# Optimization experiments

Hardware: AMD Instinct MI355X
Metric: run time of the kernel (lower is better)

The kernel has to match this reference:

```python
import jax, jax.numpy as jnp
import numpy as np


def _leaky(x):
    return jnp.where(x >= 0, x, 0.01 * x)  # nn.LeakyReLU default slope


def _conv1x1(x, w):
    # x: [B, C, H, W], w: [O, C] (1x1 conv == per-pixel channel GEMM)
    return jnp.einsum('bchw,oc->bohw', x, w)


def setup_inputs() -> dict:
    key = jax.random.key(0)
    ks = jax.random.split(key, 12)

    def kaiming(k, o, c):  # kaiming_normal_ fan_out, relu gain, 1x1 kernel
        return jax.random.normal(k, (o, c), jnp.float32) * np.float32(np.sqrt(2.0 / o))

    lr_feature = jax.random.normal(ks[0], (1, 32, 256, 512), jnp.float32)
    hr_feature = jax.random.normal(ks[1], (1, 32, 512, 1024), jnp.float32)
    return {
        'lr_feature': lr_feature,
        'hr_feature': hr_feature,
        's1_w0': kaiming(ks[2], 128, 128),
        's1_w1': kaiming(ks[3], 64, 128),
        's1_w2': kaiming(ks[4], 32, 64),
        's1_w3': kaiming(ks[5], 16, 32),
        's1_w4': kaiming(ks[6], 8, 16),
        's1_w5': kaiming(ks[7], 1, 8),
        's2_w0': kaiming(ks[8], 3, 3),
        's2_w1': kaiming(ks[9], 2, 3),
        's2_w2': kaiming(ks[10], 1, 2),
        'fuse_w': jnp.ones((1, 2), jnp.float32),  # fuse weight initialized to 1
    }


def reference(lr_feature, hr_feature, s1_w0, s1_w1, s1_w2, s1_w3, s1_w4, s1_w5,
              s2_w0, s2_w1, s2_w2, fuse_w):
    scale = hr_feature.shape[-1] // lr_feature.shape[-1]  # static python int (=2, even)
    Hh, Wh = hr_feature.shape[-2], hr_feature.shape[-1]

    # nearest-neighbor upsample of lr_feature by `scale` (expand/view trick in torch)
    lr_up = jnp.repeat(jnp.repeat(lr_feature, scale, axis=2), scale, axis=3)

    # representation: [B, 128, Hh, Wh]
    rep = jnp.concatenate(
        [lr_up, hr_feature, lr_up * hr_feature, (lr_up - hr_feature) ** 2], axis=1)

    # similarity_measure1: 1x1-conv MLP chain 128->128->64->32->16->8->1
    o = _leaky(_conv1x1(rep, s1_w0))
    o = _leaky(_conv1x1(o, s1_w1))
    o = _leaky(_conv1x1(o, s1_w2))
    o = _leaky(_conv1x1(o, s1_w3))
    o = _conv1x1(o, s1_w4)
    weights1 = _conv1x1(o, s1_w5)  # [B, 1, Hh, Wh]

    # distance matrix (even-scale branch): 3 channels [dx, dy, norm]
    v = jnp.arange(-(scale // 2), scale // 2 + 1, dtype=jnp.float32)
    m = v.shape[0] // 2
    v = jnp.concatenate([v[:m], v[m + 1:]])  # drop center -> length `scale`
    d0 = jnp.broadcast_to(v[None, :], (scale, scale))
    dm = jnp.stack([d0, d0.T, jnp.sqrt(d0 ** 2 + d0.T ** 2)], axis=0)  # [3,s,s]
    dm = jnp.tile(dm, (1, Hh // scale, Wh // scale))[None]  # [1, 3, Hh, Wh]

    # similarity_measure2: 3->3->2->1
    w2 = _leaky(_conv1x1(dm, s2_w0))
    w2 = _leaky(_conv1x1(w2, s2_w1))
    weights2 = _conv1x1(w2, s2_w2)  # [1, 1, Hh, Wh]

    # fuse (weight forced non-negative via abs, as in forward's .data mutation)
    mapping = _conv1x1(jnp.concatenate([weights1, weights2], axis=1), jnp.abs(fuse_w))
    return mapping
```

## Files before the change

kernel.cpp:

```cpp
#include <hip/hip_runtime.h>

typedef short v8s __attribute__((ext_vector_type(8)));
typedef float v4f __attribute__((ext_vector_type(4)));
typedef unsigned v4u __attribute__((ext_vector_type(4)));

#define Wh   1024
#define Hh   512
#define HWh  (Wh * Hh)
#define Wlr  512
#define HWlr (Wlr * 256)
#define ITERS 4
#define NBLK  1024

#define WFRAG_SHORTS (53 * 512)
#define LDS_BYTES    (WFRAG_SHORTS * 2)

__device__ __forceinline__ unsigned short f2bf(float f) {
    union { float f; unsigned u; } v; v.f = f;
    unsigned r = v.u + 0x7FFFu + ((v.u >> 16) & 1u);
    return (unsigned short)(r >> 16);
}
__device__ __forceinline__ unsigned pk2(float a, float b) {
    union { float f; unsigned u; } ua, ub;
    ua.f = a; ub.f = b;
    return __builtin_amdgcn_perm(ub.u + 0x8000u, ua.u + 0x8000u, 0x07060302u);
}
__device__ __forceinline__ float leaky(float x) { return fmaxf(x, 0.01f * x); }

__device__ __forceinline__ v8s relay(v4f e, v4f o) {
    v4u w;
    w[0] = pk2(leaky(e[0]), leaky(e[1]));
    w[1] = pk2(leaky(e[2]), leaky(e[3]));
    w[2] = pk2(leaky(o[0]), leaky(o[1]));
    w[3] = pk2(leaky(o[2]), leaky(o[3]));
    return __builtin_bit_cast(v8s, w);
}

__global__ __launch_bounds__(512, 2)
void cmfsm_kernel(const float* __restrict__ lr, const float* __restrict__ hr,
                  const float* __restrict__ w0g, const float* __restrict__ w1g,
                  const float* __restrict__ w2g, const float* __restrict__ w3g,
                  const float* __restrict__ w4g, const float* __restrict__ w5g,
                  const float* __restrict__ t0g, const float* __restrict__ t1g,
                  const float* __restrict__ t2g, const float* __restrict__ fwg,
                  float* __restrict__ out)
{
    extern __shared__ unsigned short smem[];
    unsigned short* wfrag = smem;

    const int tid  = threadIdx.x;
    const int lane = tid & 63;
    const int wv   = tid >> 6;
    const int p    = lane & 15;
    const int q    = lane >> 4;

    for (int e = tid; e < 32 * 64; e += 512) {
        int f = e >> 6, l = e & 63;
        int mt = f >> 2, ks = f & 3, pp = l & 15, qq = l >> 4;
        const float* src = w0g + (mt * 16 + pp) * 128 + ks * 32 + qq * 8;
        unsigned short* dst = wfrag + f * 512 + l * 8;
#pragma unroll
        for (int j = 0; j < 8; ++j) dst[j] = f2bf(src[j]);
    }
    for (int e = tid; e < 16 * 64; e += 512) {
        int f = e >> 6, l = e & 63;
        int mt = f >> 2, ks = f & 3, pp = l & 15, qq = l >> 4;
        const float* srcrow = w1g + (mt * 16 + pp) * 128;
        unsigned short* dst = wfrag + (32 + f) * 512 + l * 8;
#pragma unroll
        for (int j = 0; j < 8; ++j)
            dst[j] = f2bf(srcrow[ks * 32 + ((j >> 2) << 4) + qq * 4 + (j & 3)]);
    }
    if (tid < 4 * 64) {
        int f = tid >> 6, l = tid & 63;
        int mt = f >> 1, ks = f & 1, pp = l & 15, qq = l >> 4;
        const float* srcrow = w2g + (mt * 16 + pp) * 64;
        unsigned short* dst = wfrag + (48 + f) * 512 + l * 8;
#pragma unroll
        for (int j = 0; j < 8; ++j)
            dst[j] = f2bf(srcrow[ks * 32 + ((j >> 2) << 4) + qq * 4 + (j & 3)]);
    }
    if (tid < 64) {
        int l = tid;
        int pp = l & 15, qq = l >> 4;
        const float* srcrow = w3g + pp * 32;
        unsigned short* dst = wfrag + 52 * 512 + l * 8;
#pragma unroll
        for (int j = 0; j < 8; ++j)
            dst[j] = f2bf(srcrow[((j >> 2) << 4) + qq * 4 + (j & 3)]);
    }

    float w45[4];
#pragma unroll
    for (int r = 0; r < 4; ++r) {
        float s = 0.f;
#pragma unroll
        for (int j = 0; j < 8; ++j) s += w5g[j] * w4g[j * 16 + q * 4 + r];
        w45[r] = s;
    }

    const int row  = blockIdx.x >> 1;
    const int half = blockIdx.x & 1;

    float w2e, w2o;
    {
        float tab[4];
#pragma unroll
        for (int yp = 0; yp < 2; ++yp)
#pragma unroll
            for (int xp = 0; xp < 2; ++xp) {
                float i0 = xp ? 1.f : -1.f;
                float i1 = yp ? 1.f : -1.f;
                float i2 = 1.41421356237309505f;
                float h0[3], h1[2];
                for (int o = 0; o < 3; ++o)
                    h0[o] = leaky(t0g[o*3+0]*i0 + t0g[o*3+1]*i1 + t0g[o*3+2]*i2);
                for (int o = 0; o < 2; ++o)
                    h1[o] = leaky(t1g[o*3+0]*h0[0] + t1g[o*3+1]*h0[1] + t1g[o*3+2]*h0[2]);
                tab[yp*2+xp] = t2g[0]*h1[0] + t2g[1]*h1[1];
            }
        const int yp = row & 1;
        w2e = yp ? tab[2] : tab[0];
        w2o = yp ? tab[3] : tab[1];
    }
    const float fa = fabsf(fwg[0]);
    const float fb = fabsf(fwg[1]);

    __syncthreads();

    const unsigned short* WL = wfrag + lane * 8;

    const float* hrp[8];
    const float* lrp[8];
    {
        const int hbase = row * Wh + half * 512 + wv * 16 + p;
        const int lbase = (row >> 1) * Wlr + half * 256 + wv * 8 + (p >> 1);
#pragma unroll
        for (int j = 0; j < 8; ++j) {
            hrp[j] = hr + (size_t)(q * 8 + j) * HWh  + hbase;
            lrp[j] = lr + (size_t)(q * 8 + j) * HWlr + lbase;
        }
    }

    const v8s a3 = *(const v8s*)(WL + 52 * 512);

    const int obase = row * Wh + half * 512 + wv * 16 + p;

    float h[8], l[8];
#pragma unroll
    for (int j = 0; j < 8; ++j) { h[j] = hrp[j][0]; l[j] = lrp[j][0]; }

#pragma unroll
    for (int it = 0; it < ITERS; ++it) {
        v4u bf0, bf1, bf2, bf3;
#pragma unroll
        for (int u = 0; u < 4; ++u) {
            float l0 = l[2*u], l1 = l[2*u+1];
            float h0 = h[2*u], h1 = h[2*u+1];
            bf0[u] = pk2(l0, l1);
            bf1[u] = pk2(h0, h1);
            bf2[u] = pk2(l0 * h0, l1 * h1);
            float d0 = l0 - h0, d1 = l1 - h1;
            bf3[u] = pk2(d0 * d0, d1 * d1);
        }
        v8s b0 = __builtin_bit_cast(v8s, bf0);
        v8s b1 = __builtin_bit_cast(v8s, bf1);
        v8s b2 = __builtin_bit_cast(v8s, bf2);
        v8s b3 = __builtin_bit_cast(v8s, bf3);

        if (it + 1 < ITERS) {
            const int ho = (it + 1) * 128;
            const int lo = (it + 1) * 64;
#pragma unroll
            for (int j = 0; j < 8; ++j) {
                h[j] = hrp[j][ho];
                l[j] = lrp[j][lo];
            }
        }

        v8s c1[4];
#pragma unroll
        for (int ksp = 0; ksp < 4; ++ksp) {
            v4f ae = (v4f){0.f, 0.f, 0.f, 0.f};
            v4f ao = (v4f){0.f, 0.f, 0.f, 0.f};
#pragma unroll
            for (int ks = 0; ks < 4; ++ks) {
                v8s b = (ks == 0) ? b0 : (ks == 1) ? b1 : (ks == 2) ? b2 : b3;
                v8s we = *(const v8s*)(WL + ((2 * ksp)     * 4 + ks) * 512);
                v8s wo = *(const v8s*)(WL + ((2 * ksp + 1) * 4 + ks) * 512);
                ae = __builtin_amdgcn_mfma_f32_16x16x32_bf16(we, b, ae, 0, 0, 0);
                ao = __builtin_amdgcn_mfma_f32_16x16x32_bf16(wo, b, ao, 0, 0, 0);
            }
            c1[ksp] = relay(ae, ao);
        }

        v8s c2[2];
#pragma unroll
        for (int ksp = 0; ksp < 2; ++ksp) {
            v4f ae = (v4f){0.f, 0.f, 0.f, 0.f};
            v4f ao = (v4f){0.f, 0.f, 0.f, 0.f};
#pragma unroll
            for (int ks = 0; ks < 4; ++ks) {
                v8s we = *(const v8s*)(WL + (32 + (2 * ksp)     * 4 + ks) * 512);
                v8s wo = *(const v8s*)(WL + (32 + (2 * ksp + 1) * 4 + ks) * 512);
                ae = __builtin_amdgcn_mfma_f32_16x16x32_bf16(we, c1[ks], ae, 0, 0, 0);
                ao = __builtin_amdgcn_mfma_f32_16x16x32_bf16(wo, c1[ks], ao, 0, 0, 0);
            }
            c2[ksp] = relay(ae, ao);
        }

        v8s c3;
        {
            v4f ae = (v4f){0.f, 0.f, 0.f, 0.f};
            v4f ao = (v4f){0.f, 0.f, 0.f, 0.f};
#pragma unroll
            for (int ks = 0; ks < 2; ++ks) {
                v8s we = *(const v8s*)(WL + (48 +     ks) * 512);
                v8s wo = *(const v8s*)(WL + (48 + 2 + ks) * 512);
                ae = __builtin_amdgcn_mfma_f32_16x16x32_bf16(we, c2[ks], ae, 0, 0, 0);
                ao = __builtin_amdgcn_mfma_f32_16x16x32_bf16(wo, c2[ks], ao, 0, 0, 0);
            }
            c3 = relay(ae, ao);
        }

        {
            v4f acc3 = __builtin_amdgcn_mfma_f32_16x16x32_bf16(a3, c3, (v4f){0.f, 0.f, 0.f, 0.f}, 0, 0, 0);

            float part = 0.f;
#pragma unroll
            for (int r = 0; r < 4; ++r) part += w45[r] * leaky(acc3[r]);
            part += __shfl_xor(part, 16, 64);
            part += __shfl_xor(part, 32, 64);

            if (q == 0) {
                const float w2v = (p & 1) ? w2o : w2e;
                out[obase + it * 128] = fa * part + fb * w2v;
            }
        }
    }
}

extern "C" void kernel_launch(void* const* d_in, const int* in_sizes, int n_in,
                              void* d_out, int out_size, void* d_ws, size_t ws_size,
                              hipStream_t stream) {
    const float* lr  = (const float*)d_in[0];
    const float* hr  = (const float*)d_in[1];
    const float* w0g = (const float*)d_in[2];
    const float* w1g = (const float*)d_in[3];
    const float* w2g = (const float*)d_in[4];
    const float* w3g = (const float*)d_in[5];
    const float* w4g = (const float*)d_in[6];
    const float* w5g = (const float*)d_in[7];
    const float* t0g = (const float*)d_in[8];
    const float* t1g = (const float*)d_in[9];
    const float* t2g = (const float*)d_in[10];
    const float* fwg = (const float*)d_in[11];
    float* out = (float*)d_out;

    hipLaunchKernelGGL(cmfsm_kernel, dim3(NBLK), dim3(512), LDS_BYTES, stream,
                       lr, hr, w0g, w1g, w2g, w3g, w4g, w5g, t0g, t1g, t2g, fwg, out);
}
```

Before: 153.9 us.

## Pre-pack bf16 weight fragments in a prep kernel and copy them into LDS

Adds a small prep kernel that converts the four weight matrices to bf16 MFMA fragment layout once into workspace. The main kernel then bulk-copies 48 fragments into LDS with uint4 loads instead of every block re-converting scattered fp32 weights, and keeps the layer-2 and layer-3 fragments in registers. This shrinks LDS per block and may raise occupancy. It also replaces the manual bf16 pack with the hardware v_cvt_pk_bf16_f32 instruction, which rounds to nearest-even, and adds a second kernel launch plus extra register pressure.

```diff
diff --git a/kernel.cpp b/kernel.cpp
--- a/kernel.cpp
+++ b/kernel.cpp
@@ -13,7 +13,8 @@
 #define NBLK  1024
 
 #define WFRAG_SHORTS (53 * 512)
-#define LDS_BYTES    (WFRAG_SHORTS * 2)
+#define LDS_FRAGS    48
+#define LDS_BYTES    (LDS_FRAGS * 1024)
 
 __device__ __forceinline__ unsigned short f2bf(float f) {
     union { float f; unsigned u; } v; v.f = f;
@@ -21,9 +22,9 @@
     return (unsigned short)(r >> 16);
 }
 __device__ __forceinline__ unsigned pk2(float a, float b) {
-    union { float f; unsigned u; } ua, ub;
-    ua.f = a; ub.f = b;
-    return __builtin_amdgcn_perm(ub.u + 0x8000u, ua.u + 0x8000u, 0x07060302u);
+    unsigned r;
+    asm("v_cvt_pk_bf16_f32 %0, %1, %2" : "=v"(r) : "v"(a), "v"(b));
+    return r;
 }
 __device__ __forceinline__ float leaky(float x) { return fmaxf(x, 0.01f * x); }
 
@@ -36,10 +37,43 @@
     return __builtin_bit_cast(v8s, w);
 }
 
+__global__ void prep_kernel(const float* __restrict__ w0g, const float* __restrict__ w1g,
+                            const float* __restrict__ w2g, const float* __restrict__ w3g,
+                            unsigned short* __restrict__ ws)
+{
+    const int f = blockIdx.x;
+    const int l = threadIdx.x;
+    const int pp = l & 15, qq = l >> 4;
+    unsigned short* dst = ws + f * 512 + l * 8;
+
+    if (f < 32) {
+        int mt = f >> 2, ks = f & 3;
+        const float* src = w0g + (mt * 16 + pp) * 128 + ks * 32 + qq * 8;
+#pragma unroll
+        for (int j = 0; j < 8; ++j) dst[j] = f2bf(src[j]);
+    } else if (f < 48) {
+        int g = f - 32, mt = g >> 2, ks = g & 3;
+        const float* srcrow = w1g + (mt * 16 + pp) * 128;
+#pragma unroll
+        for (int j = 0; j < 8; ++j)
+            dst[j] = f2bf(srcrow[ks * 32 + ((j >> 2) << 4) + qq * 4 + (j & 3)]);
+    } else if (f < 52) {
+        int g = f - 48, mt = g >> 1, ks = g & 1;
+        const float* srcrow = w2g + (mt * 16 + pp) * 64;
+#pragma unroll
+        for (int j = 0; j < 8; ++j)
+            dst[j] = f2bf(srcrow[ks * 32 + ((j >> 2) << 4) + qq * 4 + (j & 3)]);
+    } else {
+        const float* srcrow = w3g + pp * 32;
+#pragma unroll
+        for (int j = 0; j < 8; ++j)
+            dst[j] = f2bf(srcrow[((j >> 2) << 4) + qq * 4 + (j & 3)]);
+    }
+}
+
 __global__ __launch_bounds__(512, 2)
 void cmfsm_kernel(const float* __restrict__ lr, const float* __restrict__ hr,
-                  const float* __restrict__ w0g, const float* __restrict__ w1g,
-                  const float* __restrict__ w2g, const float* __restrict__ w3g,
+                  const unsigned short* __restrict__ ws,
                   const float* __restrict__ w4g, const float* __restrict__ w5g,
                   const float* __restrict__ t0g, const float* __restrict__ t1g,
                   const float* __restrict__ t2g, const float* __restrict__ fwg,
@@ -54,40 +88,11 @@
     const int p    = lane & 15;
     const int q    = lane >> 4;
 
-    for (int e = tid; e < 32 * 64; e += 512) {
-        int f = e >> 6, l = e & 63;
-        int mt = f >> 2, ks = f & 3, pp = l & 15, qq = l >> 4;
-        const float* src = w0g + (mt * 16 + pp) * 128 + ks * 32 + qq * 8;
-        unsigned short* dst = wfrag + f * 512 + l * 8;
-#pragma unroll
-        for (int j = 0; j < 8; ++j) dst[j] = f2bf(src[j]);
-    }
-    for (int e = tid; e < 16 * 64; e += 512) {
-        int f = e >> 6, l = e & 63;
-        int mt = f >> 2, ks = f & 3, pp = l & 15, qq = l >> 4;
-        const float* srcrow = w1g + (mt * 16 + pp) * 128;
-        unsigned short* dst = wfrag + (32 + f) * 512 + l * 8;
-#pragma unroll
-        for (int j = 0; j < 8; ++j)
-            dst[j] = f2bf(srcrow[ks * 32 + ((j >> 2) << 4) + qq * 4 + (j & 3)]);
-    }
-    if (tid < 4 * 64) {
-        int f = tid >> 6, l = tid & 63;
-        int mt = f >> 1, ks = f & 1, pp = l & 15, qq = l >> 4;
-        const float* srcrow = w2g + (mt * 16 + pp) * 64;
-        unsigned short* dst = wfrag + (48 + f) * 512 + l * 8;
-#pragma unroll
-        for (int j = 0; j < 8; ++j)
-            dst[j] = f2bf(srcrow[ks * 32 + ((j >> 2) << 4) + qq * 4 + (j & 3)]);
-    }
-    if (tid < 64) {
-        int l = tid;
-        int pp = l & 15, qq = l >> 4;
-        const float* srcrow = w3g + pp * 32;
-        unsigned short* dst = wfrag + 52 * 512 + l * 8;
-#pragma unroll
-        for (int j = 0; j < 8; ++j)
-            dst[j] = f2bf(srcrow[((j >> 2) << 4) + qq * 4 + (j & 3)]);
+    {
+        const uint4* src = (const uint4*)ws;
+        uint4* dst = (uint4*)smem;
+#pragma unroll
+        for (int e = 0; e < 6; ++e) dst[tid + e * 512] = src[tid + e * 512];
     }
 
     float w45[4];
@@ -126,6 +131,12 @@
     const float fa = fabsf(fwg[0]);
     const float fb = fabsf(fwg[1]);
 
+    const v8s a2w[4] = {
+        *(const v8s*)(ws + 48 * 512 + lane * 8), *(const v8s*)(ws + 49 * 512 + lane * 8),
+        *(const v8s*)(ws + 50 * 512 + lane * 8), *(const v8s*)(ws + 51 * 512 + lane * 8)
+    };
+    const v8s a3 = *(const v8s*)(ws + 52 * 512 + lane * 8);
+
     __syncthreads();
 
     const unsigned short* WL = wfrag + lane * 8;
@@ -141,8 +152,6 @@
             lrp[j] = lr + (size_t)(q * 8 + j) * HWlr + lbase;
         }
     }
-
-    const v8s a3 = *(const v8s*)(WL + 52 * 512);
 
     const int obase = row * Wh + half * 512 + wv * 16 + p;
 
@@ -215,10 +224,8 @@
             v4f ao = (v4f){0.f, 0.f, 0.f, 0.f};
 #pragma unroll
             for (int ks = 0; ks < 2; ++ks) {
-                v8s we = *(const v8s*)(WL + (48 +     ks) * 512);
-                v8s wo = *(const v8s*)(WL + (48 + 2 + ks) * 512);
-                ae = __builtin_amdgcn_mfma_f32_16x16x32_bf16(we, c2[ks], ae, 0, 0, 0);
-                ao = __builtin_amdgcn_mfma_f32_16x16x32_bf16(wo, c2[ks], ao, 0, 0, 0);
+                ae = __builtin_amdgcn_mfma_f32_16x16x32_bf16(a2w[ks],     c2[ks], ae, 0, 0, 0);
+                ao = __builtin_amdgcn_mfma_f32_16x16x32_bf16(a2w[2 + ks], c2[ks], ao, 0, 0, 0);
             }
             c3 = relay(ae, ao);
         }
@@ -256,7 +263,10 @@
     const float* t2g = (const float*)d_in[10];
     const float* fwg = (const float*)d_in[11];
     float* out = (float*)d_out;
-
+    unsigned short* ws = (unsigned short*)d_ws;
+
+    hipLaunchKernelGGL(prep_kernel, dim3(53), dim3(64), 0, stream,
+                       w0g, w1g, w2g, w3g, ws);
     hipLaunchKernelGGL(cmfsm_kernel, dim3(NBLK), dim3(512), LDS_BYTES, stream,
-                       lr, hr, w0g, w1g, w2g, w3g, w4g, w5g, t0g, t1g, t2g, fwg, out);
-}
+                       lr, hr, ws, w4g, w5g, t0g, t1g, t2g, fwg, out);
+}
```

New measurement: 145.8 us. -5.3%, faster.
